# Optimization experiments

Measured on AMD Instinct MI355X. Metric: run time of the kernel, lower is better.

The kernel has to match this reference:

```python
import jax, jax.numpy as jnp
import numpy as np

N, E, G = 50000, 800000, 256
H, C = 8, 16
F0 = 64
FH = H * C  # 128
L = 6
EPS = 1e-5
SEL = [0, 1, 2, 3, 4, 5, 5, 5]  # <10 layers -> pad with last


def setup_inputs() -> dict:
    key = jax.random.key(0)
    ks = jax.random.split(key, 32)

    def w(k, shape, fan_in):
        return jax.random.normal(k, shape, jnp.float32) / np.float32(np.sqrt(fan_in))

    inp = {
        'x': jax.random.normal(ks[0], (N, F0), jnp.float32),
        'edge_index': jax.random.randint(ks[1], (2, E), 0, N),
        'batch_vec': jnp.sort(jax.random.randint(ks[2], (N,), 0, G)),
        # layer 0 (in=F0)
        'Wq0': w(ks[3], (F0, FH), F0), 'bq0': 0.01 * jax.random.normal(ks[4], (FH,), jnp.float32),
        'Wk0': w(ks[5], (F0, FH), F0), 'bk0': 0.01 * jax.random.normal(ks[6], (FH,), jnp.float32),
        'Wv0': w(ks[7], (F0, FH), F0), 'bv0': 0.01 * jax.random.normal(ks[8], (FH,), jnp.float32),
        'Ws0': w(ks[9], (F0, FH), F0), 'bs0': 0.01 * jax.random.normal(ks[10], (FH,), jnp.float32),
        # layers 1..L-1 (in=FH), stacked
        'Wq': w(ks[11], (L - 1, FH, FH), FH), 'bq': 0.01 * jax.random.normal(ks[12], (L - 1, FH), jnp.float32),
        'Wk': w(ks[13], (L - 1, FH, FH), FH), 'bk': 0.01 * jax.random.normal(ks[14], (L - 1, FH), jnp.float32),
        'Wv': w(ks[15], (L - 1, FH, FH), FH), 'bv': 0.01 * jax.random.normal(ks[16], (L - 1, FH), jnp.float32),
        'Ws': w(ks[17], (L - 1, FH, FH), FH), 'bs': 0.01 * jax.random.normal(ks[18], (L - 1, FH), jnp.float32),
        # BatchNorm affine params per layer
        'gamma': jnp.ones((L, FH), jnp.float32),
        'beta': jnp.zeros((L, FH), jnp.float32),
    }
    return inp


def _transformer_conv(x, src, dst, Wq, bq, Wk, bk, Wv, bv, Ws, bs):
    # q from target nodes, k/v from source nodes (PyG TransformerConv, concat=True)
    q = (x @ Wq + bq).reshape(-1, H, C)
    k = (x @ Wk + bk).reshape(-1, H, C)
    v = (x @ Wv + bv).reshape(-1, H, C)
    s = jnp.einsum('ehc,ehc->eh', q[dst], k[src]) * np.float32(1.0 / np.sqrt(C))  # [E,H]
    m = jax.ops.segment_max(s, dst, num_segments=N)       # segment softmax over in-edges
    e = jnp.exp(s - m[dst])
    denom = jax.ops.segment_sum(e, dst, num_segments=N)
    alpha = e / jnp.maximum(denom[dst], 1e-16)            # [E,H]
    msg = jax.ops.segment_sum(alpha[:, :, None] * v[src], dst, num_segments=N)  # [N,H,C]
    return msg.reshape(-1, FH) + (x @ Ws + bs)            # root/skip connection


def _bn_relu(x, g, b):
    mu = jnp.mean(x, axis=0)
    var = jnp.var(x, axis=0)  # biased, as used for normalization in training mode
    return jax.nn.relu((x - mu) * jax.lax.rsqrt(var + EPS) * g + b)


def reference(x, edge_index, batch_vec, Wq0, bq0, Wk0, bk0, Wv0, bv0, Ws0, bs0,
              Wq, bq, Wk, bk, Wv, bv, Ws, bs, gamma, beta):
    src, dst = edge_index[0], edge_index[1]
    outs = []
    h = _bn_relu(_transformer_conv(x, src, dst, Wq0, bq0, Wk0, bk0, Wv0, bv0, Ws0, bs0),
                 gamma[0], beta[0])
    outs.append(h)
    for i in range(L - 1):
        h = _bn_relu(_transformer_conv(h, src, dst, Wq[i], bq[i], Wk[i], bk[i],
                                       Wv[i], bv[i], Ws[i], bs[i]),
                     gamma[i + 1], beta[i + 1])
        outs.append(h)
    counts = jnp.maximum(jax.ops.segment_sum(jnp.ones((N,), x.dtype), batch_vec, num_segments=G), 1.0)
    pooled = [jax.ops.segment_sum(o, batch_vec, num_segments=G) / counts[:, None] for o in outs]
    latent = jnp.stack([pooled[i] for i in SEL], axis=1)  # [G, 8, FH]
    return latent.reshape(G, -1)                          # [G, 8*FH]
```

## Files before the change

kernel.cpp:

```cpp
#include <hip/hip_runtime.h>
#include <hip/hip_bf16.h>
#include <math.h>

#define NN 50000
#define NE 800000
#define NG 256
#define FHH 128
#define NL 6
#define NCH 49
#define NB 391

typedef __attribute__((ext_vector_type(8))) short s16x8;
typedef __attribute__((ext_vector_type(4))) float f32x4;

__device__ __forceinline__ ushort f2bf(float x) {
  uint u = __float_as_uint(x);
  u += 0x7fffu + ((u >> 16) & 1u);
  return (ushort)(u >> 16);
}
__device__ __forceinline__ float bf2f(ushort h) {
  return __uint_as_float(((uint)h) << 16);
}
__device__ __forceinline__ float bfl(uint u) { return __uint_as_float(u << 16); }
__device__ __forceinline__ float bfh(uint u) { return __uint_as_float(u & 0xffff0000u); }

__device__ __forceinline__ void gload16(const ushort* g, ushort* l) {
  __builtin_amdgcn_global_load_lds(
      (const __attribute__((address_space(1))) uint*)(const void*)g,
      (__attribute__((address_space(3))) uint*)(void*)l, 16, 0, 0);
}

__global__ void k_gstart(const int* __restrict__ bv, int* __restrict__ gstart) {
  int g = blockIdx.x * blockDim.x + threadIdx.x;
  if (g > NG) return;
  int lo = 0, hi = NN;
  while (lo < hi) { int mid = (lo + hi) >> 1; if (bv[mid] < g) lo = mid + 1; else hi = mid; }
  gstart[g] = lo;
}

__global__ void k_deg(const int* __restrict__ dstv, int* __restrict__ deg) {
  int e = blockIdx.x * blockDim.x + threadIdx.x;
  if (e < NE) atomicAdd(&deg[dstv[e]], 1);
}

__global__ __launch_bounds__(256) void k_scanA(const int* __restrict__ deg, int* __restrict__ part) {
  int b = blockIdx.x, t = threadIdx.x;
  int s = 0;
  for (int j = t; j < 1024; j += 256) { int i = b * 1024 + j; if (i < NN) s += deg[i]; }
  __shared__ int sh[4];
  for (int o = 32; o; o >>= 1) s += __shfl_down(s, o, 64);
  if ((t & 63) == 0) sh[t >> 6] = s;
  __syncthreads();
  if (t == 0) part[b] = sh[0] + sh[1] + sh[2] + sh[3];
}

__global__ void k_scanB(int* __restrict__ part, int* __restrict__ row_ptr) {
  if (threadIdx.x == 0 && blockIdx.x == 0) {
    int run = 0;
    for (int i = 0; i < NCH; ++i) { int v = part[i]; part[i] = run; run += v; }
    row_ptr[NN] = run;
  }
}

__global__ __launch_bounds__(1024) void k_scanC(const int* __restrict__ deg, const int* __restrict__ part,
                                                int* __restrict__ row_ptr, int* __restrict__ cursor) {
  __shared__ int buf[1024];
  int b = blockIdx.x, t = threadIdx.x;
  int i = b * 1024 + t;
  int v = (i < NN) ? deg[i] : 0;
  buf[t] = v;
  __syncthreads();
  for (int off = 1; off < 1024; off <<= 1) {
    int add = (t >= off) ? buf[t - off] : 0;
    __syncthreads();
    buf[t] += add;
    __syncthreads();
  }
  if (i < NN) { int ex = part[b] + buf[t] - v; row_ptr[i] = ex; cursor[i] = ex; }
}

__global__ void k_scatter(const int* __restrict__ srcv, const int* __restrict__ dstv,
                          int* __restrict__ cursor, int* __restrict__ col) {
  int e = blockIdx.x * blockDim.x + threadIdx.x;
  if (e < NE) {
    int d = dstv[e];
    int pos = atomicAdd(&cursor[d], 1);
    col[pos] = srcv[e];
  }
}

__device__ __forceinline__ size_t wtile_idx(int k, int c) {
  return (size_t)(k >> 5) * 4096 + ((((c >> 4) * 4 + ((k & 31) >> 3)) * 16 + (c & 15)) * 8 + (k & 7));
}

__global__ __launch_bounds__(256) void k_wconv0(const float* __restrict__ W0, const float* __restrict__ W1,
                                                const float* __restrict__ W2, const float* __restrict__ W3,
                                                ushort* __restrict__ wh, ushort* __restrict__ wl) {
  int id = blockIdx.x * 256 + threadIdx.x;
  if (id >= 4 * 64 * 128) return;
  int mat = id >> 13, rem = id & 8191;
  int k = rem >> 7, c = rem & 127;
  const float* W = (mat == 0) ? W0 : (mat == 1) ? W1 : (mat == 2) ? W2 : W3;
  float v = W[k * 128 + c];
  ushort h = f2bf(v);
  ushort lo = f2bf(v - bf2f(h));
  size_t dst = (size_t)mat * 8192 + wtile_idx(k, c);
  wh[dst] = h; wl[dst] = lo;
}

__global__ __launch_bounds__(256) void k_wconvS(const float* __restrict__ Wq, const float* __restrict__ Wk,
                                                const float* __restrict__ Wv, const float* __restrict__ Ws,
                                                ushort* __restrict__ wh, ushort* __restrict__ wl) {
  int id = blockIdx.x * 256 + threadIdx.x;
  if (id >= 5 * 4 * 16384) return;
  int lay = id / 65536, rem = id % 65536;
  int mat = rem >> 14, rem2 = rem & 16383;
  int k = rem2 >> 7, c = rem2 & 127;
  const float* W = (mat == 0) ? Wq : (mat == 1) ? Wk : (mat == 2) ? Wv : Ws;
  float v = W[(size_t)lay * 16384 + k * 128 + c];
  ushort h = f2bf(v);
  ushort lo = f2bf(v - bf2f(h));
  size_t dst = 32768 + ((size_t)lay * 4 + mat) * 16384 + wtile_idx(k, c);
  wh[dst] = h; wl[dst] = lo;
}

template <int K>
__global__ __launch_bounds__(256) void k_presplit(const float* __restrict__ Y, int use_bn,
                                                  const float* __restrict__ sums,
                                                  const float* __restrict__ sumsq,
                                                  const float* __restrict__ gvec,
                                                  const float* __restrict__ bvec,
                                                  ushort* __restrict__ Xh, ushort* __restrict__ Xl) {
  const int CP = K / 4;
  int idx = blockIdx.x * 256 + threadIdx.x;
  int row = idx / CP;
  int c4 = (idx % CP) * 4;
  if (row >= NN) return;
  float4 v = *reinterpret_cast<const float4*>(Y + (size_t)row * K + c4);
  if (use_bn) {
    const float invn = 1.f / (float)NN;
    float4 s4 = *reinterpret_cast<const float4*>(sums + c4);
    float4 q4 = *reinterpret_cast<const float4*>(sumsq + c4);
    float4 g4 = *reinterpret_cast<const float4*>(gvec + c4);
    float4 b4 = *reinterpret_cast<const float4*>(bvec + c4);
    float mu, var, sc, sh;
    mu = s4.x * invn; var = q4.x * invn - mu * mu; sc = g4.x * rsqrtf(var + 1e-5f); sh = b4.x - mu * sc;
    v.x = fmaxf(fmaf(v.x, sc, sh), 0.f);
    mu = s4.y * invn; var = q4.y * invn - mu * mu; sc = g4.y * rsqrtf(var + 1e-5f); sh = b4.y - mu * sc;
    v.y = fmaxf(fmaf(v.y, sc, sh), 0.f);
    mu = s4.z * invn; var = q4.z * invn - mu * mu; sc = g4.z * rsqrtf(var + 1e-5f); sh = b4.z - mu * sc;
    v.z = fmaxf(fmaf(v.z, sc, sh), 0.f);
    mu = s4.w * invn; var = q4.w * invn - mu * mu; sc = g4.w * rsqrtf(var + 1e-5f); sh = b4.w - mu * sc;
    v.w = fmaxf(fmaf(v.w, sc, sh), 0.f);
  }
  ushort h0 = f2bf(v.x), h1 = f2bf(v.y), h2 = f2bf(v.z), h3 = f2bf(v.w);
  ushort l0 = f2bf(v.x - bf2f(h0)), l1 = f2bf(v.y - bf2f(h1));
  ushort l2 = f2bf(v.z - bf2f(h2)), l3 = f2bf(v.w - bf2f(h3));
  int b = row >> 7, g = (row & 127) >> 4, frow = row & 15;
  int ks = c4 >> 5, qq = (c4 & 31) >> 3, j = c4 & 7;
  size_t base = ((size_t)ks * NB + b) * 4096 + (((g * 4 + qq) * 16) + frow) * 8 + j;
  *reinterpret_cast<uint2*>(Xh + base) =
      make_uint2((uint)h0 | ((uint)h1 << 16), (uint)h2 | ((uint)h3 << 16));
  *reinterpret_cast<uint2*>(Xl + base) =
      make_uint2((uint)l0 | ((uint)l1 << 16), (uint)l2 | ((uint)l3 << 16));
}

template <int K>
__global__ __launch_bounds__(256, 2) void k_gemm(
    const ushort* __restrict__ Xh, const ushort* __restrict__ Xl,
    const ushort* __restrict__ Wth, const ushort* __restrict__ Wtl,
    const float* __restrict__ b0, const float* __restrict__ b1,
    const float* __restrict__ b2, const float* __restrict__ b3,
    float* __restrict__ Yq, ushort* __restrict__ kv, float* __restrict__ Yxs) {
  __shared__ __align__(16) ushort Ah[4096];
  __shared__ __align__(16) ushort Al[4096];
  __shared__ __align__(16) ushort Bh[4096];
  __shared__ __align__(16) ushort Bl[4096];
  int t = threadIdx.x;
  int lane = t & 63, w = t >> 6;
  int wr = w >> 1, wc = w & 1;
  int frow = lane & 15;
  int mat = blockIdx.y;
  const ushort* wh = Wth + (size_t)mat * (K * 128);
  const ushort* wl = Wtl + (size_t)mat * (K * 128);
  const float* bb = (mat == 0) ? b0 : (mat == 1) ? b1 : (mat == 2) ? b2 : b3;

  f32x4 acc[4][4];
#pragma unroll
  for (int i = 0; i < 4; ++i)
#pragma unroll
    for (int j = 0; j < 4; ++j)
#pragma unroll
      for (int r = 0; r < 4; ++r) acc[i][j][r] = 0.f;

  int wofs = w * 1024 + lane * 8;
  for (int ks = 0; ks < K / 32; ++ks) {
    size_t abase = ((size_t)ks * NB + blockIdx.x) * 4096;
    const ushort* gAh = Xh + abase + wofs;
    const ushort* gAl = Xl + abase + wofs;
    const ushort* gBh = wh + ks * 4096 + wofs;
    const ushort* gBl = wl + ks * 4096 + wofs;
    gload16(gAh, &Ah[w * 1024]);
    gload16(gAh + 512, &Ah[w * 1024 + 512]);
    gload16(gAl, &Al[w * 1024]);
    gload16(gAl + 512, &Al[w * 1024 + 512]);
    gload16(gBh, &Bh[w * 1024]);
    gload16(gBh + 512, &Bh[w * 1024 + 512]);
    gload16(gBl, &Bl[w * 1024]);
    gload16(gBl + 512, &Bl[w * 1024 + 512]);
    __syncthreads();
    s16x8 ah[4], al[4], bh[4], bl[4];
#pragma unroll
    for (int g = 0; g < 4; ++g) {
      ah[g] = *reinterpret_cast<const s16x8*>(&Ah[(wr * 4 + g) * 512 + lane * 8]);
      al[g] = *reinterpret_cast<const s16x8*>(&Al[(wr * 4 + g) * 512 + lane * 8]);
      bh[g] = *reinterpret_cast<const s16x8*>(&Bh[(wc * 4 + g) * 512 + lane * 8]);
      bl[g] = *reinterpret_cast<const s16x8*>(&Bl[(wc * 4 + g) * 512 + lane * 8]);
    }
#pragma unroll
    for (int rg = 0; rg < 4; ++rg)
#pragma unroll
      for (int cg = 0; cg < 4; ++cg) {
        acc[rg][cg] = __builtin_amdgcn_mfma_f32_16x16x32_bf16(ah[rg], bh[cg], acc[rg][cg], 0, 0, 0);
        acc[rg][cg] = __builtin_amdgcn_mfma_f32_16x16x32_bf16(al[rg], bh[cg], acc[rg][cg], 0, 0, 0);
        acc[rg][cg] = __builtin_amdgcn_mfma_f32_16x16x32_bf16(ah[rg], bl[cg], acc[rg][cg], 0, 0, 0);
      }
    __syncthreads();
  }
  int r0 = blockIdx.x * 128;
  int qq = (lane >> 4) << 2;
#pragma unroll
  for (int rg = 0; rg < 4; ++rg) {
#pragma unroll
    for (int cg = 0; cg < 4; ++cg) {
      int colg = wc * 64 + cg * 16 + frow;
      float bv = bb[colg];
#pragma unroll
      for (int r = 0; r < 4; ++r) {
        int row = r0 + wr * 64 + rg * 16 + qq + r;
        if (row >= NN) continue;
        float val = acc[rg][cg][r] + bv;
        if (mat == 0)      Yq [(size_t)row * FHH + colg] = val;
        else if (mat == 3) Yxs[(size_t)row * FHH + colg] = val;
        else {
          int pos = (colg >> 1) * 4 + ((mat == 2) ? 2 : 0) + (colg & 1);
          kv[(size_t)row * 256 + pos] = f2bf(val);
        }
      }
    }
  }
}

__global__ __launch_bounds__(128) void k_agg(const float* __restrict__ q,
                                             const ushort* __restrict__ kv,
                                             const float* __restrict__ xs,
                                             const int* __restrict__ row_ptr,
                                             const int* __restrict__ col,
                                             float* __restrict__ y) {
  int n = blockIdx.x * 2 + (threadIdx.x >> 6);
  int t = threadIdx.x & 63;
  float2 qf = *reinterpret_cast<const float2*>(q + (size_t)n * FHH + 2 * t);
  const uint2* kvp = reinterpret_cast<const uint2*>(kv);
  int e0 = row_ptr[n], e1 = row_ptr[n + 1];
  float m = -INFINITY, sum = 0.f, a0 = 0.f, a1 = 0.f;
  int i = e0;
  for (; i + 4 <= e1; i += 4) {
    int s0 = col[i], s1 = col[i + 1], s2 = col[i + 2], s3 = col[i + 3];
    uint2 d0 = kvp[((size_t)s0 << 6) + t];
    uint2 d1 = kvp[((size_t)s1 << 6) + t];
    uint2 d2 = kvp[((size_t)s2 << 6) + t];
    uint2 d3 = kvp[((size_t)s3 << 6) + t];
    float p0 = fmaf(qf.x, bfl(d0.x), qf.y * bfh(d0.x));
    float p1 = fmaf(qf.x, bfl(d1.x), qf.y * bfh(d1.x));
    float p2 = fmaf(qf.x, bfl(d2.x), qf.y * bfh(d2.x));
    float p3 = fmaf(qf.x, bfl(d3.x), qf.y * bfh(d3.x));
    p0 += __shfl_xor(p0, 1, 8); p1 += __shfl_xor(p1, 1, 8);
    p2 += __shfl_xor(p2, 1, 8); p3 += __shfl_xor(p3, 1, 8);
    p0 += __shfl_xor(p0, 2, 8); p1 += __shfl_xor(p1, 2, 8);
    p2 += __shfl_xor(p2, 2, 8); p3 += __shfl_xor(p3, 2, 8);
    p0 += __shfl_xor(p0, 4, 8); p1 += __shfl_xor(p1, 4, 8);
    p2 += __shfl_xor(p2, 4, 8); p3 += __shfl_xor(p3, 4, 8);
    float sc0 = p0 * 0.25f, sc1 = p1 * 0.25f, sc2 = p2 * 0.25f, sc3 = p3 * 0.25f;
    float nm = fmaxf(m, fmaxf(fmaxf(sc0, sc1), fmaxf(sc2, sc3)));
    float r = __expf(m - nm);
    float w0 = __expf(sc0 - nm), w1 = __expf(sc1 - nm);
    float w2 = __expf(sc2 - nm), w3 = __expf(sc3 - nm);
    sum = fmaf(sum, r, (w0 + w1) + (w2 + w3));
    a0 = fmaf(a0, r, fmaf(w0, bfl(d0.y), fmaf(w1, bfl(d1.y), fmaf(w2, bfl(d2.y), w3 * bfl(d3.y)))));
    a1 = fmaf(a1, r, fmaf(w0, bfh(d0.y), fmaf(w1, bfh(d1.y), fmaf(w2, bfh(d2.y), w3 * bfh(d3.y)))));
    m = nm;
  }
  for (; i < e1; ++i) {
    int s0 = col[i];
    uint2 d0 = kvp[((size_t)s0 << 6) + t];
    float p0 = fmaf(qf.x, bfl(d0.x), qf.y * bfh(d0.x));
    p0 += __shfl_xor(p0, 1, 8);
    p0 += __shfl_xor(p0, 2, 8);
    p0 += __shfl_xor(p0, 4, 8);
    float sc0 = p0 * 0.25f;
    float nm = fmaxf(m, sc0);
    float r = __expf(m - nm);
    float w0 = __expf(sc0 - nm);
    sum = fmaf(sum, r, w0);
    a0 = fmaf(a0, r, w0 * bfl(d0.y));
    a1 = fmaf(a1, r, w0 * bfh(d0.y));
    m = nm;
  }
  float inv = 1.f / fmaxf(sum, 1e-16f);
  float2 xv = *reinterpret_cast<const float2*>(xs + (size_t)n * FHH + 2 * t);
  float2 ov;
  ov.x = fmaf(a0, inv, xv.x);
  ov.y = fmaf(a1, inv, xv.y);
  *reinterpret_cast<float2*>(y + (size_t)n * FHH + 2 * t) = ov;
}

__global__ __launch_bounds__(256) void k_bnstats(const float* __restrict__ y,
                                                 float* __restrict__ sums,
                                                 float* __restrict__ sumsq) {
  __shared__ float s1[256], s2[256];
  int f = threadIdx.x & 127;
  int half = threadIdx.x >> 7;
  float a = 0.f, b = 0.f;
  for (int r = blockIdx.x * 2 + half; r < NN; r += 512) {
    float val = y[(size_t)r * FHH + f];
    a += val;
    b += val * val;
  }
  s1[threadIdx.x] = a;
  s2[threadIdx.x] = b;
  __syncthreads();
  if (half == 0) {
    a += s1[threadIdx.x + 128];
    b += s2[threadIdx.x + 128];
    atomicAdd(&sums[f], a);
    atomicAdd(&sumsq[f], b);
  }
}

__global__ __launch_bounds__(128) void k_pool(const float* __restrict__ y,
                                              const float* __restrict__ sums,
                                              const float* __restrict__ sumsq,
                                              const float* __restrict__ gvec,
                                              const float* __restrict__ bvec,
                                              const int* __restrict__ gstart,
                                              float* __restrict__ out, int layer) {
  int g = blockIdx.x;
  int part = blockIdx.y;
  int f = threadIdx.x;
  const float invn = 1.f / (float)NN;
  float mu = sums[f] * invn;
  float var = sumsq[f] * invn - mu * mu;
  float sc = gvec[f] * rsqrtf(var + 1e-5f);
  float sh = bvec[f] - mu * sc;
  int r0 = gstart[g], r1 = gstart[g + 1];
  int len = r1 - r0;
  int q0 = r0 + (len * part) / 4;
  int q1 = r0 + (len * (part + 1)) / 4;
  float s = 0.f;
  for (int r = q0; r < q1; ++r) s += fmaxf(fmaf(y[(size_t)r * FHH + f], sc, sh), 0.f);
  float p = s / (float)(len > 0 ? len : 1);
  if (layer < 5) {
    atomicAdd(&out[(size_t)g * 1024 + layer * FHH + f], p);
  } else {
    atomicAdd(&out[(size_t)g * 1024 + 5 * FHH + f], p);
    atomicAdd(&out[(size_t)g * 1024 + 6 * FHH + f], p);
    atomicAdd(&out[(size_t)g * 1024 + 7 * FHH + f], p);
  }
}

extern "C" void kernel_launch(void* const* d_in, const int* in_sizes, int n_in,
                              void* d_out, int out_size, void* d_ws, size_t ws_size,
                              hipStream_t stream) {
  (void)in_sizes; (void)n_in; (void)ws_size;
  const float* x    = (const float*)d_in[0];
  const int*   ei   = (const int*)d_in[1];
  const int*   bvec = (const int*)d_in[2];
  const float* Wq0  = (const float*)d_in[3];
  const float* bq0  = (const float*)d_in[4];
  const float* Wk0  = (const float*)d_in[5];
  const float* bk0  = (const float*)d_in[6];
  const float* Wv0  = (const float*)d_in[7];
  const float* bv0  = (const float*)d_in[8];
  const float* Ws0  = (const float*)d_in[9];
  const float* bs0  = (const float*)d_in[10];
  const float* WqS  = (const float*)d_in[11];
  const float* bqS  = (const float*)d_in[12];
  const float* WkS  = (const float*)d_in[13];
  const float* bkS  = (const float*)d_in[14];
  const float* WvS  = (const float*)d_in[15];
  const float* bvS  = (const float*)d_in[16];
  const float* WsS  = (const float*)d_in[17];
  const float* bsS  = (const float*)d_in[18];
  const float* gamma = (const float*)d_in[19];
  const float* beta  = (const float*)d_in[20];
  float* out = (float*)d_out;

  char* ws = (char*)d_ws;
  size_t off = 0;
  auto alloc = [&](size_t bytes) {
    void* p = ws + off;
    off = (off + bytes + 255) & ~(size_t)255;
    return p;
  };
  float* q    = (float*)alloc((size_t)NN * FHH * 4);
  float* xs   = (float*)alloc((size_t)NN * FHH * 4);
  float* y    = (float*)alloc((size_t)NN * FHH * 4);
  ushort* kv  = (ushort*)alloc((size_t)NN * 256 * 2);
  ushort* Xh  = (ushort*)alloc((size_t)4 * NB * 4096 * 2 + 8192);
  ushort* Xl  = (ushort*)alloc((size_t)4 * NB * 4096 * 2 + 8192);
  int* col     = (int*)alloc((size_t)NE * 4);
  int* row_ptr = (int*)alloc((size_t)(NN + 1) * 4);
  int* cursor  = (int*)alloc((size_t)NN * 4);
  int* deg     = (int*)alloc((size_t)NN * 4);
  int* part    = (int*)alloc((size_t)NCH * 4);
  int* gstart  = (int*)alloc((size_t)(NG + 1) * 4);
  float* bstat = (float*)alloc((size_t)NL * 2 * FHH * 4);
  ushort* wsh = (ushort*)alloc((size_t)360448 * 2);
  ushort* wsl = (ushort*)alloc((size_t)360448 * 2);

  const int* srcv = ei;
  const int* dstv = ei + NE;

  hipMemsetAsync(out, 0, (size_t)out_size * 4, stream);
  hipMemsetAsync(deg, 0, (size_t)NN * 4, stream);
  hipMemsetAsync(bstat, 0, (size_t)NL * 2 * FHH * 4, stream);
  k_gstart<<<5, 64, 0, stream>>>(bvec, gstart);
  k_deg<<<(NE + 255) / 256, 256, 0, stream>>>(dstv, deg);
  k_scanA<<<NCH, 256, 0, stream>>>(deg, part);
  k_scanB<<<1, 64, 0, stream>>>(part, row_ptr);
  k_scanC<<<NCH, 1024, 0, stream>>>(deg, part, row_ptr, cursor);
  k_scatter<<<(NE + 255) / 256, 256, 0, stream>>>(srcv, dstv, cursor, col);
  k_wconv0<<<128, 256, 0, stream>>>(Wq0, Wk0, Wv0, Ws0, wsh, wsl);
  k_wconvS<<<1280, 256, 0, stream>>>(WqS, WkS, WvS, WsS, wsh, wsl);
  k_presplit<64><<<(NN * 16 + 255) / 256, 256, 0, stream>>>(x, 0, nullptr, nullptr,
                                                            nullptr, nullptr, Xh, Xl);

  for (int l = 0; l < NL; ++l) {
    const ushort* WthL = wsh + ((l == 0) ? 0 : (size_t)32768 + (size_t)(l - 1) * 65536);
    const ushort* WtlL = wsl + ((l == 0) ? 0 : (size_t)32768 + (size_t)(l - 1) * 65536);
    const float *bq_, *bk_, *bv_, *bs_;
    if (l == 0) { bq_ = bq0; bk_ = bk0; bv_ = bv0; bs_ = bs0; }
    else {
      size_t bo = (size_t)(l - 1) * FHH;
      bq_ = bqS + bo; bk_ = bkS + bo; bv_ = bvS + bo; bs_ = bsS + bo;
    }
    dim3 gg(NB, 4);
    if (l == 0)
      k_gemm<64><<<gg, 256, 0, stream>>>(Xh, Xl, WthL, WtlL, bq_, bk_, bv_, bs_, q, kv, xs);
    else
      k_gemm<128><<<gg, 256, 0, stream>>>(Xh, Xl, WthL, WtlL, bq_, bk_, bv_, bs_, q, kv, xs);
    k_agg<<<NN / 2, 128, 0, stream>>>(q, kv, xs, row_ptr, col, y);
    float* lsum = bstat + (size_t)l * 2 * FHH;
    float* lsqs = lsum + FHH;
    k_bnstats<<<256, 256, 0, stream>>>(y, lsum, lsqs);
    dim3 pg2(NG, 4);
    k_pool<<<pg2, FHH, 0, stream>>>(y, lsum, lsqs, gamma + (size_t)l * FHH,
                                    beta + (size_t)l * FHH, gstart, out, l);
    if (l + 1 < NL)
      k_presplit<128><<<(NN * 32 + 255) / 256, 256, 0, stream>>>(
          y, 1, lsum, lsqs, gamma + (size_t)l * FHH, beta + (size_t)l * FHH, Xh, Xl);
  }
}
```

Measured before the change: 1.119 ms.

## Fuse BN pooling with presplit, store q as scaled bf16, drop online-max softmax

Merges the per-graph pooling kernel with the BN+ReLU+bf16-split kernel so y is read once per layer, and pools eight rows per block with atomics. The GEMM now writes q as bf16 prescaled by log2(e)/sqrt(C), so the aggregation reads half the q bytes and uses exp2 directly. The online max subtraction is removed in favour of a clamped exp2. Column indices are stored as prescaled byte offsets. Skipping the max subtraction risks overflow or precision loss if scores grow large, and q loses precision going to bf16.

```diff
diff --git a/kernel.cpp b/kernel.cpp
--- a/kernel.cpp
+++ b/kernel.cpp
@@ -12,6 +12,8 @@
 
 typedef __attribute__((ext_vector_type(8))) short s16x8;
 typedef __attribute__((ext_vector_type(4))) float f32x4;
+
+#define QSCALE 0.36067376022224085f
 
 __device__ __forceinline__ ushort f2bf(float x) {
   uint u = __float_as_uint(x);
@@ -80,12 +82,12 @@
 }
 
 __global__ void k_scatter(const int* __restrict__ srcv, const int* __restrict__ dstv,
-                          int* __restrict__ cursor, int* __restrict__ col) {
+                          int* __restrict__ cursor, uint* __restrict__ colb) {
   int e = blockIdx.x * blockDim.x + threadIdx.x;
   if (e < NE) {
     int d = dstv[e];
     int pos = atomicAdd(&cursor[d], 1);
-    col[pos] = srcv[e];
+    colb[pos] = ((uint)srcv[e]) << 9;
   }
 }
 
@@ -125,11 +127,7 @@
 }
 
 template <int K>
-__global__ __launch_bounds__(256) void k_presplit(const float* __restrict__ Y, int use_bn,
-                                                  const float* __restrict__ sums,
-                                                  const float* __restrict__ sumsq,
-                                                  const float* __restrict__ gvec,
-                                                  const float* __restrict__ bvec,
+__global__ __launch_bounds__(256) void k_presplit(const float* __restrict__ Y,
                                                   ushort* __restrict__ Xh, ushort* __restrict__ Xl) {
   const int CP = K / 4;
   int idx = blockIdx.x * 256 + threadIdx.x;
@@ -137,22 +135,6 @@
   int c4 = (idx % CP) * 4;
   if (row >= NN) return;
   float4 v = *reinterpret_cast<const float4*>(Y + (size_t)row * K + c4);
-  if (use_bn) {
-    const float invn = 1.f / (float)NN;
-    float4 s4 = *reinterpret_cast<const float4*>(sums + c4);
-    float4 q4 = *reinterpret_cast<const float4*>(sumsq + c4);
-    float4 g4 = *reinterpret_cast<const float4*>(gvec + c4);
-    float4 b4 = *reinterpret_cast<const float4*>(bvec + c4);
-    float mu, var, sc, sh;
-    mu = s4.x * invn; var = q4.x * invn - mu * mu; sc = g4.x * rsqrtf(var + 1e-5f); sh = b4.x - mu * sc;
-    v.x = fmaxf(fmaf(v.x, sc, sh), 0.f);
-    mu = s4.y * invn; var = q4.y * invn - mu * mu; sc = g4.y * rsqrtf(var + 1e-5f); sh = b4.y - mu * sc;
-    v.y = fmaxf(fmaf(v.y, sc, sh), 0.f);
-    mu = s4.z * invn; var = q4.z * invn - mu * mu; sc = g4.z * rsqrtf(var + 1e-5f); sh = b4.z - mu * sc;
-    v.z = fmaxf(fmaf(v.z, sc, sh), 0.f);
-    mu = s4.w * invn; var = q4.w * invn - mu * mu; sc = g4.w * rsqrtf(var + 1e-5f); sh = b4.w - mu * sc;
-    v.w = fmaxf(fmaf(v.w, sc, sh), 0.f);
-  }
   ushort h0 = f2bf(v.x), h1 = f2bf(v.y), h2 = f2bf(v.z), h3 = f2bf(v.w);
   ushort l0 = f2bf(v.x - bf2f(h0)), l1 = f2bf(v.y - bf2f(h1));
   ushort l2 = f2bf(v.z - bf2f(h2)), l3 = f2bf(v.w - bf2f(h3));
@@ -171,7 +153,7 @@
     const ushort* __restrict__ Wth, const ushort* __restrict__ Wtl,
     const float* __restrict__ b0, const float* __restrict__ b1,
     const float* __restrict__ b2, const float* __restrict__ b3,
-    float* __restrict__ Yq, ushort* __restrict__ kv, float* __restrict__ Yxs) {
+    ushort* __restrict__ qbf, ushort* __restrict__ kv, float* __restrict__ Yxs) {
   __shared__ __align__(16) ushort Ah[4096];
   __shared__ __align__(16) ushort Al[4096];
   __shared__ __align__(16) ushort Bh[4096];
@@ -240,7 +222,7 @@
         int row = r0 + wr * 64 + rg * 16 + qq + r;
         if (row >= NN) continue;
         float val = acc[rg][cg][r] + bv;
-        if (mat == 0)      Yq [(size_t)row * FHH + colg] = val;
+        if (mat == 0)      qbf[(size_t)row * FHH + colg] = f2bf(val * QSCALE);
         else if (mat == 3) Yxs[(size_t)row * FHH + colg] = val;
         else {
           int pos = (colg >> 1) * 4 + ((mat == 2) ? 2 : 0) + (colg & 1);
@@ -251,67 +233,64 @@
   }
 }
 
-__global__ __launch_bounds__(128) void k_agg(const float* __restrict__ q,
+__global__ __launch_bounds__(256) void k_agg(const uint* __restrict__ qb,
                                              const ushort* __restrict__ kv,
                                              const float* __restrict__ xs,
                                              const int* __restrict__ row_ptr,
-                                             const int* __restrict__ col,
+                                             const uint* __restrict__ colb,
                                              float* __restrict__ y) {
-  int n = blockIdx.x * 2 + (threadIdx.x >> 6);
+  int n = blockIdx.x * 4 + (threadIdx.x >> 6);
   int t = threadIdx.x & 63;
-  float2 qf = *reinterpret_cast<const float2*>(q + (size_t)n * FHH + 2 * t);
-  const uint2* kvp = reinterpret_cast<const uint2*>(kv);
+  uint qp = qb[(n << 6) + t];
+  float qx = bfl(qp), qy = bfh(qp);
+  const char* kvb = (const char*)kv;
+  uint tof = (uint)t * 8u;
   int e0 = row_ptr[n], e1 = row_ptr[n + 1];
-  float m = -INFINITY, sum = 0.f, a0 = 0.f, a1 = 0.f;
+  float sum = 0.f, a0 = 0.f, a1 = 0.f;
   int i = e0;
   for (; i + 4 <= e1; i += 4) {
-    int s0 = col[i], s1 = col[i + 1], s2 = col[i + 2], s3 = col[i + 3];
-    uint2 d0 = kvp[((size_t)s0 << 6) + t];
-    uint2 d1 = kvp[((size_t)s1 << 6) + t];
-    uint2 d2 = kvp[((size_t)s2 << 6) + t];
-    uint2 d3 = kvp[((size_t)s3 << 6) + t];
-    float p0 = fmaf(qf.x, bfl(d0.x), qf.y * bfh(d0.x));
-    float p1 = fmaf(qf.x, bfl(d1.x), qf.y * bfh(d1.x));
-    float p2 = fmaf(qf.x, bfl(d2.x), qf.y * bfh(d2.x));
-    float p3 = fmaf(qf.x, bfl(d3.x), qf.y * bfh(d3.x));
+    uint o0 = colb[i] + tof, o1 = colb[i + 1] + tof;
+    uint o2 = colb[i + 2] + tof, o3 = colb[i + 3] + tof;
+    uint2 d0 = *(const uint2*)(kvb + o0);
+    uint2 d1 = *(const uint2*)(kvb + o1);
+    uint2 d2 = *(const uint2*)(kvb + o2);
+    uint2 d3 = *(const uint2*)(kvb + o3);
+    float p0 = fmaf(qx, bfl(d0.x), qy * bfh(d0.x));
+    float p1 = fmaf(qx, bfl(d1.x), qy * bfh(d1.x));
+    float p2 = fmaf(qx, bfl(d2.x), qy * bfh(d2.x));
+    float p3 = fmaf(qx, bfl(d3.x), qy * bfh(d3.x));
     p0 += __shfl_xor(p0, 1, 8); p1 += __shfl_xor(p1, 1, 8);
     p2 += __shfl_xor(p2, 1, 8); p3 += __shfl_xor(p3, 1, 8);
     p0 += __shfl_xor(p0, 2, 8); p1 += __shfl_xor(p1, 2, 8);
     p2 += __shfl_xor(p2, 2, 8); p3 += __shfl_xor(p3, 2, 8);
     p0 += __shfl_xor(p0, 4, 8); p1 += __shfl_xor(p1, 4, 8);
     p2 += __shfl_xor(p2, 4, 8); p3 += __shfl_xor(p3, 4, 8);
-    float sc0 = p0 * 0.25f, sc1 = p1 * 0.25f, sc2 = p2 * 0.25f, sc3 = p3 * 0.25f;
-    float nm = fmaxf(m, fmaxf(fmaxf(sc0, sc1), fmaxf(sc2, sc3)));
-    float r = __expf(m - nm);
-    float w0 = __expf(sc0 - nm), w1 = __expf(sc1 - nm);
-    float w2 = __expf(sc2 - nm), w3 = __expf(sc3 - nm);
-    sum = fmaf(sum, r, (w0 + w1) + (w2 + w3));
-    a0 = fmaf(a0, r, fmaf(w0, bfl(d0.y), fmaf(w1, bfl(d1.y), fmaf(w2, bfl(d2.y), w3 * bfl(d3.y)))));
-    a1 = fmaf(a1, r, fmaf(w0, bfh(d0.y), fmaf(w1, bfh(d1.y), fmaf(w2, bfh(d2.y), w3 * bfh(d3.y)))));
-    m = nm;
+    float w0 = exp2f(fminf(p0, 110.f));
+    float w1 = exp2f(fminf(p1, 110.f));
+    float w2 = exp2f(fminf(p2, 110.f));
+    float w3 = exp2f(fminf(p3, 110.f));
+    sum += (w0 + w1) + (w2 + w3);
+    a0 = fmaf(w0, bfl(d0.y), fmaf(w1, bfl(d1.y), fmaf(w2, bfl(d2.y), fmaf(w3, bfl(d3.y), a0))));
+    a1 = fmaf(w0, bfh(d0.y), fmaf(w1, bfh(d1.y), fmaf(w2, bfh(d2.y), fmaf(w3, bfh(d3.y), a1))));
   }
   for (; i < e1; ++i) {
-    int s0 = col[i];
-    uint2 d0 = kvp[((size_t)s0 << 6) + t];
-    float p0 = fmaf(qf.x, bfl(d0.x), qf.y * bfh(d0.x));
+    uint o0 = colb[i] + tof;
+    uint2 d0 = *(const uint2*)(kvb + o0);
+    float p0 = fmaf(qx, bfl(d0.x), qy * bfh(d0.x));
     p0 += __shfl_xor(p0, 1, 8);
     p0 += __shfl_xor(p0, 2, 8);
     p0 += __shfl_xor(p0, 4, 8);
-    float sc0 = p0 * 0.25f;
-    float nm = fmaxf(m, sc0);
-    float r = __expf(m - nm);
-    float w0 = __expf(sc0 - nm);
-    sum = fmaf(sum, r, w0);
-    a0 = fmaf(a0, r, w0 * bfl(d0.y));
-    a1 = fmaf(a1, r, w0 * bfh(d0.y));
-    m = nm;
+    float w0 = exp2f(fminf(p0, 110.f));
+    sum += w0;
+    a0 = fmaf(w0, bfl(d0.y), a0);
+    a1 = fmaf(w0, bfh(d0.y), a1);
   }
   float inv = 1.f / fmaxf(sum, 1e-16f);
-  float2 xv = *reinterpret_cast<const float2*>(xs + (size_t)n * FHH + 2 * t);
+  float2 xv = *reinterpret_cast<const float2*>(xs + ((size_t)n << 7) + 2 * t);
   float2 ov;
   ov.x = fmaf(a0, inv, xv.x);
   ov.y = fmaf(a1, inv, xv.y);
-  *reinterpret_cast<float2*>(y + (size_t)n * FHH + 2 * t) = ov;
+  *reinterpret_cast<float2*>(y + ((size_t)n << 7) + 2 * t) = ov;
 }
 
 __global__ __launch_bounds__(256) void k_bnstats(const float* __restrict__ y,
@@ -337,34 +316,84 @@
   }
 }
 
-__global__ __launch_bounds__(128) void k_pool(const float* __restrict__ y,
+template <int WRITE_X>
+__global__ __launch_bounds__(256) void k_post(const float* __restrict__ y,
                                               const float* __restrict__ sums,
                                               const float* __restrict__ sumsq,
                                               const float* __restrict__ gvec,
-                                              const float* __restrict__ bvec,
+                                              const float* __restrict__ bvec_,
+                                              const int* __restrict__ bv,
                                               const int* __restrict__ gstart,
-                                              float* __restrict__ out, int layer) {
-  int g = blockIdx.x;
-  int part = blockIdx.y;
-  int f = threadIdx.x;
-  const float invn = 1.f / (float)NN;
-  float mu = sums[f] * invn;
-  float var = sumsq[f] * invn - mu * mu;
-  float sc = gvec[f] * rsqrtf(var + 1e-5f);
-  float sh = bvec[f] - mu * sc;
-  int r0 = gstart[g], r1 = gstart[g + 1];
-  int len = r1 - r0;
-  int q0 = r0 + (len * part) / 4;
-  int q1 = r0 + (len * (part + 1)) / 4;
-  float s = 0.f;
-  for (int r = q0; r < q1; ++r) s += fmaxf(fmaf(y[(size_t)r * FHH + f], sc, sh), 0.f);
-  float p = s / (float)(len > 0 ? len : 1);
-  if (layer < 5) {
-    atomicAdd(&out[(size_t)g * 1024 + layer * FHH + f], p);
-  } else {
-    atomicAdd(&out[(size_t)g * 1024 + 5 * FHH + f], p);
-    atomicAdd(&out[(size_t)g * 1024 + 6 * FHH + f], p);
-    atomicAdd(&out[(size_t)g * 1024 + 7 * FHH + f], p);
+                                              float* __restrict__ out, int layer,
+                                              ushort* __restrict__ Xh, ushort* __restrict__ Xl) {
+  __shared__ float acts[8][128];
+  __shared__ int sg[8];
+  __shared__ float ssc[128], ssh[128];
+  int b = blockIdx.x, t = threadIdx.x;
+  if (t < 128) {
+    const float invn = 1.f / (float)NN;
+    float mu = sums[t] * invn;
+    float var = sumsq[t] * invn - mu * mu;
+    float sc = gvec[t] * rsqrtf(var + 1e-5f);
+    ssc[t] = sc;
+    ssh[t] = bvec_[t] - mu * sc;
+  }
+  if (t < 8) sg[t] = (b * 8 + t < NN) ? bv[b * 8 + t] : -1;
+  __syncthreads();
+  int row = b * 8 + (t >> 5);
+  int c4 = (t & 31) * 4;
+  bool ok = row < NN;
+  float4 a = make_float4(0.f, 0.f, 0.f, 0.f);
+  if (ok) {
+    float4 v = *reinterpret_cast<const float4*>(y + (size_t)row * FHH + c4);
+    a.x = fmaxf(fmaf(v.x, ssc[c4 + 0], ssh[c4 + 0]), 0.f);
+    a.y = fmaxf(fmaf(v.y, ssc[c4 + 1], ssh[c4 + 1]), 0.f);
+    a.z = fmaxf(fmaf(v.z, ssc[c4 + 2], ssh[c4 + 2]), 0.f);
+    a.w = fmaxf(fmaf(v.w, ssc[c4 + 3], ssh[c4 + 3]), 0.f);
+  }
+  *reinterpret_cast<float4*>(&acts[t >> 5][c4]) = a;
+  if (WRITE_X && ok) {
+    ushort h0 = f2bf(a.x), h1 = f2bf(a.y), h2 = f2bf(a.z), h3 = f2bf(a.w);
+    ushort l0 = f2bf(a.x - bf2f(h0)), l1 = f2bf(a.y - bf2f(h1));
+    ushort l2 = f2bf(a.z - bf2f(h2)), l3 = f2bf(a.w - bf2f(h3));
+    int bb = row >> 7, g = (row & 127) >> 4, frow = row & 15;
+    int ks = c4 >> 5, qq = (c4 & 31) >> 3, j = c4 & 7;
+    size_t base = ((size_t)ks * NB + bb) * 4096 + (((g * 4 + qq) * 16) + frow) * 8 + j;
+    *reinterpret_cast<uint2*>(Xh + base) =
+        make_uint2((uint)h0 | ((uint)h1 << 16), (uint)h2 | ((uint)h3 << 16));
+    *reinterpret_cast<uint2*>(Xl + base) =
+        make_uint2((uint)l0 | ((uint)l1 << 16), (uint)l2 | ((uint)l3 << 16));
+  }
+  __syncthreads();
+  if (t < 128) {
+    float racc = 0.f;
+    int cg = sg[0];
+    for (int r = 0; r < 8; ++r) {
+      int g = sg[r];
+      if (g != cg) {
+        if (cg >= 0) {
+          float p = racc / (float)(gstart[cg + 1] - gstart[cg]);
+          if (layer < 5) atomicAdd(&out[(size_t)cg * 1024 + layer * FHH + t], p);
+          else {
+            atomicAdd(&out[(size_t)cg * 1024 + 5 * FHH + t], p);
+            atomicAdd(&out[(size_t)cg * 1024 + 6 * FHH + t], p);
+            atomicAdd(&out[(size_t)cg * 1024 + 7 * FHH + t], p);
+          }
+        }
+        racc = 0.f;
+        cg = g;
+      }
+      racc += acts[r][t];
+    }
+    if (cg >= 0) {
+      float p = racc / (float)(gstart[cg + 1] - gstart[cg]);
+      if (layer < 5) atomicAdd(&out[(size_t)cg * 1024 + layer * FHH + t], p);
+      else {
+        atomicAdd(&out[(size_t)cg * 1024 + 5 * FHH + t], p);
+        atomicAdd(&out[(size_t)cg * 1024 + 6 * FHH + t], p);
+        atomicAdd(&out[(size_t)cg * 1024 + 7 * FHH + t], p);
+      }
+    }
   }
 }
 
@@ -402,13 +431,13 @@
     off = (off + bytes + 255) & ~(size_t)255;
     return p;
   };
-  float* q    = (float*)alloc((size_t)NN * FHH * 4);
+  ushort* qbf = (ushort*)alloc((size_t)NN * FHH * 2);
   float* xs   = (float*)alloc((size_t)NN * FHH * 4);
   float* y    = (float*)alloc((size_t)NN * FHH * 4);
   ushort* kv  = (ushort*)alloc((size_t)NN * 256 * 2);
   ushort* Xh  = (ushort*)alloc((size_t)4 * NB * 4096 * 2 + 8192);
   ushort* Xl  = (ushort*)alloc((size_t)4 * NB * 4096 * 2 + 8192);
-  int* col     = (int*)alloc((size_t)NE * 4);
+  uint* colb   = (uint*)alloc((size_t)NE * 4);
   int* row_ptr = (int*)alloc((size_t)(NN + 1) * 4);
   int* cursor  = (int*)alloc((size_t)NN * 4);
   int* deg     = (int*)alloc((size_t)NN * 4);
@@ -429,11 +458,10 @@
   k_scanA<<<NCH, 256, 0, stream>>>(deg, part);
   k_scanB<<<1, 64, 0, stream>>>(part, row_ptr);
   k_scanC<<<NCH, 1024, 0, stream>>>(deg, part, row_ptr, cursor);
-  k_scatter<<<(NE + 255) / 256, 256, 0, stream>>>(srcv, dstv, cursor, col);
+  k_scatter<<<(NE + 255) / 256, 256, 0, stream>>>(srcv, dstv, cursor, colb);
   k_wconv0<<<128, 256, 0, stream>>>(Wq0, Wk0, Wv0, Ws0, wsh, wsl);
   k_wconvS<<<1280, 256, 0, stream>>>(WqS, WkS, WvS, WsS, wsh, wsl);
-  k_presplit<64><<<(NN * 16 + 255) / 256, 256, 0, stream>>>(x, 0, nullptr, nullptr,
-                                                            nullptr, nullptr, Xh, Xl);
+  k_presplit<64><<<(NN * 16 + 255) / 256, 256, 0, stream>>>(x, Xh, Xl);
 
   for (int l = 0; l < NL; ++l) {
     const ushort* WthL = wsh + ((l == 0) ? 0 : (size_t)32768 + (size_t)(l - 1) * 65536);
@@ -446,18 +474,18 @@
     }
     dim3 gg(NB, 4);
     if (l == 0)
-      k_gemm<64><<<gg, 256, 0, stream>>>(Xh, Xl, WthL, WtlL, bq_, bk_, bv_, bs_, q, kv, xs);
+      k_gemm<64><<<gg, 256, 0, stream>>>(Xh, Xl, WthL, WtlL, bq_, bk_, bv_, bs_, qbf, kv, xs);
     else
-      k_gemm<128><<<gg, 256, 0, stream>>>(Xh, Xl, WthL, WtlL, bq_, bk_, bv_, bs_, q, kv, xs);
-    k_agg<<<NN / 2, 128, 0, stream>>>(q, kv, xs, row_ptr, col, y);
+      k_gemm<128><<<gg, 256, 0, stream>>>(Xh, Xl, WthL, WtlL, bq_, bk_, bv_, bs_, qbf, kv, xs);
+    k_agg<<<NN / 4, 256, 0, stream>>>((const uint*)qbf, kv, xs, row_ptr, colb, y);
     float* lsum = bstat + (size_t)l * 2 * FHH;
     float* lsqs = lsum + FHH;
     k_bnstats<<<256, 256, 0, stream>>>(y, lsum, lsqs);
-    dim3 pg2(NG, 4);
-    k_pool<<<pg2, FHH, 0, stream>>>(y, lsum, lsqs, gamma + (size_t)l * FHH,
-                                    beta + (size_t)l * FHH, gstart, out, l);
     if (l + 1 < NL)
-      k_presplit<128><<<(NN * 32 + 255) / 256, 256, 0, stream>>>(
-          y, 1, lsum, lsqs, gamma + (size_t)l * FHH, beta + (size_t)l * FHH, Xh, Xl);
-  }
-}
+      k_post<1><<<6250, 256, 0, stream>>>(y, lsum, lsqs, gamma + (size_t)l * FHH,
+                                          beta + (size_t)l * FHH, bvec, gstart, out, l, Xh, Xl);
+    else
+      k_post<0><<<6250, 256, 0, stream>>>(y, lsum, lsqs, gamma + (size_t)l * FHH,
+                                          beta + (size_t)l * FHH, bvec, gstart, out, l, Xh, Xl);
+  }
+}
```

New measurement: 1.019 ms. 1.1x faster.
